# Performance work log

Hardware: AMD Instinct MI355X
Metric: run time of the kernel (lower is better)

The kernel has to match this reference:

```python
import jax, jax.numpy as jnp
import numpy as np

N_NODES = 10000
N_EDGES = 640000
D_IN = 128
D_OUT = 128


def setup_inputs() -> dict:
    key = jax.random.key(0)
    k_x, k_val, k_w, k_row, k_col = jax.random.split(key, 5)
    # Glorot init for weight, zeros for bias (matches _weight_init)
    limit = float(np.sqrt(6.0 / (D_IN + D_OUT)))
    weight = jax.random.uniform(k_w, (D_IN, D_OUT), jnp.float32, -limit, limit)
    return {
        "x": jax.random.normal(k_x, (N_NODES, D_IN), jnp.float32),
        "adj_val": jax.random.uniform(k_val, (N_EDGES,), jnp.float32),  # normalized edge weights of sparse adj
        "weight": weight,
        "bias": jnp.zeros((D_OUT,), jnp.float32),
        "adj_row": jax.random.randint(k_row, (N_EDGES,), 0, N_NODES, jnp.int32),
        "adj_col": jax.random.randint(k_col, (N_EDGES,), 0, N_NODES, jnp.int32),
    }


def reference(x, adj_val, weight, bias, adj_row, adj_col):
    # dense GEMM: h = x @ W  -> [N, D_OUT]
    h = jnp.matmul(x, weight)
    # SpMM with COO adjacency: out[r] = sum_{e: row[e]=r} val[e] * h[col[e]]
    msg = adj_val[:, None] * h[adj_col]  # [E, D_OUT] gather + scale
    out = jax.ops.segment_sum(msg, adj_row, num_segments=x.shape[0])
    return out + bias
```

## Files before the change

kernel.cpp:

```cpp
#include <hip/hip_runtime.h>

#define N_NODES 10000
#define N_EDGES 640000
#define D 128
#define NQ (N_EDGES / 4)

#define NCHUNK 64
#define QPC (NQ / NCHUNK)
#define GEMM_BLOCKS 157
#define GRID1 (NCHUNK + GEMM_BLOCKS)
#define RCAP 8
#define SPILLCAP 10000
#define CAP2 128
#define QPAD2 144
#define LSTR 136

typedef unsigned int uint32;
typedef unsigned long long u64;
typedef unsigned short u16;
typedef unsigned char u8;
using short8 = __attribute__((ext_vector_type(8))) short;
using f32x4  = __attribute__((ext_vector_type(4))) float;

__device__ __forceinline__ uint32 f2bf_bits(float f) {
    uint32 u = __float_as_uint(f);
    return (u + 0x7FFFu + ((u >> 16) & 1u)) >> 16;
}
__device__ __forceinline__ uint32 pack2(float lo, float hi) {
    return f2bf_bits(lo) | (f2bf_bits(hi) << 16);
}

__global__ __launch_bounds__(256, 4) void gemm_scatter_kernel(
    const float* __restrict__ x, const float* __restrict__ w,
    const int* __restrict__ row, const int* __restrict__ col,
    const float* __restrict__ val,
    uint32* __restrict__ h2, u8* __restrict__ cnts2,
    int* __restrict__ spillcnt, uint32* __restrict__ bstore,
    uint2* __restrict__ spill)
{
    __shared__ __align__(16) int SH[N_NODES];
    __shared__ int spillc;
    const int t = threadIdx.x;

    if (blockIdx.x < NCHUNK) {
        int* hist = SH;
        for (int i = t; i < N_NODES; i += 256) hist[i] = 0;
        if (t == 0) spillc = 0;
        __syncthreads();

        const int sb = blockIdx.x;
        const int4*   row4 = (const int4*)row;
        const int4*   col4 = (const int4*)col;
        const float4* val4 = (const float4*)val;
        const int i0 = sb * QPC;
        for (int i = i0 + t; i < i0 + QPC; i += 256) {
            int4 r = row4[i]; int4 c = col4[i]; float4 v = val4[i];
            #pragma unroll
            for (int e = 0; e < 4; ++e) {
                int rr = (e == 0) ? r.x : (e == 1) ? r.y : (e == 2) ? r.z : r.w;
                int cc = (e == 0) ? c.x : (e == 1) ? c.y : (e == 2) ? c.z : c.w;
                float vv = (e == 0) ? v.x : (e == 1) ? v.y : (e == 2) ? v.z : v.w;
                uint32 rc = (uint32)cc | (f2bf_bits(vv) << 16);
                int k = atomicAdd(&hist[rr], 1);
                if (k < RCAP)
                    bstore[(size_t)rr * (NCHUNK * RCAP) + sb * RCAP + k] = rc;
                else {
                    int ks = atomicAdd(&spillc, 1);
                    spill[(size_t)sb * SPILLCAP + ks] = make_uint2(rc, (uint32)rr);
                }
            }
        }
        __syncthreads();
        for (int r = t; r < N_NODES; r += 256) {
            int c = hist[r];
            cnts2[(size_t)sb * N_NODES + r] = (u8)((c < RCAP) ? c : RCAP);
        }
        if (t == 0) spillcnt[sb] = spillc;
    } else {
        u16* Ws = (u16*)SH;
        const int g = blockIdx.x - NCHUNK;
        const int lane = t & 63;
        const int wid  = t >> 6;
        const int q = lane >> 4, cl = lane & 15;

        const float4* w4 = (const float4*)w;
        #pragma unroll
        for (int i = 0; i < 8; ++i) {
            int lin = t + i * 256;
            int m  = lin >> 5;
            int qc = lin & 31;
            float4 r0 = w4[(2 * m) * 32 + qc];
            float4 r1 = w4[(2 * m + 1) * 32 + qc];
            int c = qc * 4;
            *(uint32*)&Ws[(c + 0) * LSTR + 2 * m] = pack2(r0.x, r1.x);
            *(uint32*)&Ws[(c + 1) * LSTR + 2 * m] = pack2(r0.y, r1.y);
            *(uint32*)&Ws[(c + 2) * LSTR + 2 * m] = pack2(r0.z, r1.z);
            *(uint32*)&Ws[(c + 3) * LSTR + 2 * m] = pack2(r0.w, r1.w);
        }

        int gr = g * 64 + wid * 16 + cl;
        if (gr >= N_NODES) gr = N_NODES - 1;
        const float* xrow = &x[(size_t)gr * D];
        float4 xv[8];
        #pragma unroll
        for (int kk = 0; kk < 4; ++kk) {
            xv[2 * kk]     = *(const float4*)&xrow[kk * 32 + q * 8];
            xv[2 * kk + 1] = *(const float4*)&xrow[kk * 32 + q * 8 + 4];
        }
        __syncthreads();

        f32x4 acc[8] = {};
        #pragma unroll
        for (int kk = 0; kk < 4; ++kk) {
            union { short8 s; uint32 u[4]; } af;
            float4 a = xv[2 * kk], b = xv[2 * kk + 1];
            af.u[0] = pack2(a.x, a.y); af.u[1] = pack2(a.z, a.w);
            af.u[2] = pack2(b.x, b.y); af.u[3] = pack2(b.z, b.w);
            #pragma unroll
            for (int ct = 0; ct < 8; ++ct) {
                short8 bf = *(const short8*)&Ws[(ct * 16 + cl) * LSTR + kk * 32 + q * 8];
                acc[ct] = __builtin_amdgcn_mfma_f32_16x16x32_bf16(af.s, bf, acc[ct], 0, 0, 0);
            }
        }
        #pragma unroll
        for (int reg = 0; reg < 4; ++reg) {
            int node = g * 64 + wid * 16 + q * 4 + reg;
            if (node < N_NODES) {
                uint32* base = h2 + (size_t)node * 64 + cl;
                #pragma unroll
                for (int ct = 0; ct < 4; ++ct)
                    base[ct * 16] = pack2(acc[ct][reg], acc[ct + 4][reg]);
            }
        }
    }
}

__global__ __launch_bounds__(256) void spmm_kernel(
    const uint32* __restrict__ bstore, const u8* __restrict__ cnts2,
    const int* __restrict__ spillcnt, const uint2* __restrict__ spill,
    const uint32* __restrict__ h2, const float* __restrict__ bias,
    float* __restrict__ out)
{
    __shared__ uint32 qbuf[8 * QPAD2];
    __shared__ u64 lcnt8[NCHUNK];
    const int t = threadIdx.x;
    const int lane = t & 63;
    const int wid  = t >> 6;
    const int r0 = blockIdx.x * 8;

    if (t < NCHUNK)
        lcnt8[t] = *(const u64*)&cnts2[(size_t)t * N_NODES + r0];
    const bool anyspill = __ballot(spillcnt[lane] != 0) != 0ull;
    __syncthreads();

    for (int half = 0; half < 2; ++half) {
        const int d = wid * 2 + half;
        const int r = r0 + d;
        uint32* qp = &qbuf[d * QPAD2];

        int c = (int)((lcnt8[lane] >> (8 * d)) & 0xFFu);
        int p = c;
        #pragma unroll
        for (int s = 1; s < 64; s <<= 1) {
            int v = __shfl_up(p, s);
            if (lane >= s) p += v;
        }
        int ntot = __shfl(p, 63);
        int base = p - c;
        const uint32* cell = &bstore[(size_t)r * (NCHUNK * RCAP) + lane * RCAP];
        uint4 c0 = {0, 0, 0, 0}, c1 = {0, 0, 0, 0};
        if (c > 0) c0 = *(const uint4*)cell;
        if (c > 4) c1 = *(const uint4*)(cell + 4);
        if (c > 0 && base + 0 < CAP2) qp[base + 0] = c0.x;
        if (c > 1 && base + 1 < CAP2) qp[base + 1] = c0.y;
        if (c > 2 && base + 2 < CAP2) qp[base + 2] = c0.z;
        if (c > 3 && base + 3 < CAP2) qp[base + 3] = c0.w;
        if (c > 4 && base + 4 < CAP2) qp[base + 4] = c1.x;
        if (c > 5 && base + 5 < CAP2) qp[base + 5] = c1.y;
        if (c > 6 && base + 6 < CAP2) qp[base + 6] = c1.z;
        if (c > 7 && base + 7 < CAP2) qp[base + 7] = c1.w;

        if (anyspill) {
            for (int ch = 0; ch < NCHUNK; ++ch) {
                int sc = spillcnt[ch];
                for (int k = 0; k < sc; ++k) {
                    uint2 e = spill[(size_t)ch * SPILLCAP + k];
                    if (e.y == (uint32)r) {
                        if (lane == 0 && ntot < CAP2) qp[ntot] = e.x;
                        ntot++;
                    }
                }
            }
        }

        float a0 = 0.f, a1 = 0.f;
        if (ntot <= CAP2) {
            if (lane < 16) qp[ntot + lane] = 0;
            __builtin_amdgcn_s_waitcnt(0);

            const int npad = (ntot + 7) & ~7;
            uint32 rq0,rq1,rq2,rq3,rq4,rq5,rq6,rq7;
            uint32 hh0,hh1,hh2,hh3,hh4,hh5,hh6,hh7;
            rq0 = qp[0]; hh0 = h2[((rq0 & 0xFFFFu) << 6) + lane];
            rq1 = qp[1]; hh1 = h2[((rq1 & 0xFFFFu) << 6) + lane];
            rq2 = qp[2]; hh2 = h2[((rq2 & 0xFFFFu) << 6) + lane];
            rq3 = qp[3]; hh3 = h2[((rq3 & 0xFFFFu) << 6) + lane];
            rq4 = qp[4]; hh4 = h2[((rq4 & 0xFFFFu) << 6) + lane];
            rq5 = qp[5]; hh5 = h2[((rq5 & 0xFFFFu) << 6) + lane];
            rq6 = qp[6]; hh6 = h2[((rq6 & 0xFFFFu) << 6) + lane];
            rq7 = qp[7]; hh7 = h2[((rq7 & 0xFFFFu) << 6) + lane];

#define CONSUME_PREFETCH(RQ, HH, P)                                          \
    {                                                                        \
        a0 = fmaf(__uint_as_float(RQ & 0xFFFF0000u),                         \
                  __uint_as_float(HH << 16), a0);                            \
        a1 = fmaf(__uint_as_float(RQ & 0xFFFF0000u),                         \
                  __uint_as_float(HH & 0xFFFF0000u), a1);                    \
        uint32 rn = qp[j + 8 + P];                                           \
        RQ = rn; HH = h2[((rn & 0xFFFFu) << 6) + lane];                      \
    }

            for (int j = 0; j < npad; j += 8) {
                CONSUME_PREFETCH(rq0, hh0, 0)
                CONSUME_PREFETCH(rq1, hh1, 1)
                CONSUME_PREFETCH(rq2, hh2, 2)
                CONSUME_PREFETCH(rq3, hh3, 3)
                CONSUME_PREFETCH(rq4, hh4, 4)
                CONSUME_PREFETCH(rq5, hh5, 5)
                CONSUME_PREFETCH(rq6, hh6, 6)
                CONSUME_PREFETCH(rq7, hh7, 7)
            }
#undef CONSUME_PREFETCH
        } else {
            for (int ch = 0; ch < NCHUNK; ++ch) {
                int c2 = (int)((lcnt8[ch] >> (8 * d)) & 0xFFu);
                for (int k = 0; k < c2; ++k) {
                    uint32 rec = bstore[(size_t)r * (NCHUNK * RCAP) + ch * RCAP + k];
                    uint32 hv = h2[((rec & 0xFFFFu) << 6) + lane];
                    a0 = fmaf(__uint_as_float(rec & 0xFFFF0000u),
                              __uint_as_float(hv << 16), a0);
                    a1 = fmaf(__uint_as_float(rec & 0xFFFF0000u),
                              __uint_as_float(hv & 0xFFFF0000u), a1);
                }
            }
            for (int ch = 0; ch < NCHUNK; ++ch) {
                int sc = spillcnt[ch];
                for (int k = 0; k < sc; ++k) {
                    uint2 e = spill[(size_t)ch * SPILLCAP + k];
                    if (e.y == (uint32)r) {
                        uint32 hv = h2[((e.x & 0xFFFFu) << 6) + lane];
                        a0 = fmaf(__uint_as_float(e.x & 0xFFFF0000u),
                                  __uint_as_float(hv << 16), a0);
                        a1 = fmaf(__uint_as_float(e.x & 0xFFFF0000u),
                                  __uint_as_float(hv & 0xFFFF0000u), a1);
                    }
                }
            }
        }

        out[(size_t)r * D + lane]      = a0 + bias[lane];
        out[(size_t)r * D + 64 + lane] = a1 + bias[lane + 64];
    }
}

extern "C" void kernel_launch(void* const* d_in, const int* in_sizes, int n_in,
                              void* d_out, int out_size, void* d_ws, size_t ws_size,
                              hipStream_t stream)
{
    const float* x    = (const float*)d_in[0];
    const float* aval = (const float*)d_in[1];
    const float* w    = (const float*)d_in[2];
    const float* bias = (const float*)d_in[3];
    const int* arow   = (const int*)d_in[4];
    const int* acol   = (const int*)d_in[5];

    char* ws = (char*)d_ws;
    uint32* h2       = (uint32*)(ws);
    u8*     cnts2    = (u8*)(ws + 2560000);
    int*    spillcnt = (int*)(ws + 3200000);
    uint32* bstore   = (uint32*)(ws + 3200512);
    uint2*  spill    = (uint2*)(ws + 23680512);

    gemm_scatter_kernel<<<GRID1, 256, 0, stream>>>(
        x, w, arow, acol, aval, h2, cnts2, spillcnt, bstore, spill);
    spmm_kernel<<<N_NODES / 8, 256, 0, stream>>>(
        bstore, cnts2, spillcnt, spill, h2, bias, (float*)d_out);
}
```

Before: 107.3 us.

## Split edge bucketing into 256 chunks and have each lane gather four chunk cells

Raises the number of scatter chunks from 64 to 256, so the first kernel runs more bucketing blocks, each handling fewer edges, and per-chunk spill capacity shrinks. In the SpMM kernel each lane now reads four chunk counts and four bucket cells, sums them for the prefix scan, and compacts their records into the shared queue, while the spill check uses a vectorized count load. The aim is more parallelism and less per-block serial work in the scatter phase. The cost is a workspace that grows from about 24 MB to about 87 MB, more count and bucket reads per row, and spill fallback loops that now walk 256 chunks.

```diff
diff --git a/kernel.cpp b/kernel.cpp
--- a/kernel.cpp
+++ b/kernel.cpp
@@ -5,12 +5,12 @@
 #define D 128
 #define NQ (N_EDGES / 4)
 
-#define NCHUNK 64
+#define NCHUNK 256
 #define QPC (NQ / NCHUNK)
 #define GEMM_BLOCKS 157
 #define GRID1 (NCHUNK + GEMM_BLOCKS)
 #define RCAP 8
-#define SPILLCAP 10000
+#define SPILLCAP 2500
 #define CAP2 128
 #define QPAD2 144
 #define LSTR 136
@@ -148,9 +148,9 @@
     const int wid  = t >> 6;
     const int r0 = blockIdx.x * 8;
 
-    if (t < NCHUNK)
-        lcnt8[t] = *(const u64*)&cnts2[(size_t)t * N_NODES + r0];
-    const bool anyspill = __ballot(spillcnt[lane] != 0) != 0ull;
+    lcnt8[t] = *(const u64*)&cnts2[(size_t)t * N_NODES + r0];
+    const int4 s4 = ((const int4*)spillcnt)[lane];
+    const bool anyspill = __ballot((s4.x | s4.y | s4.z | s4.w) != 0) != 0ull;
     __syncthreads();
 
     for (int half = 0; half < 2; ++half) {
@@ -158,7 +158,11 @@
         const int r = r0 + d;
         uint32* qp = &qbuf[d * QPAD2];
 
-        int c = (int)((lcnt8[lane] >> (8 * d)) & 0xFFu);
+        int c0 = (int)((lcnt8[lane * 4 + 0] >> (8 * d)) & 0xFFu);
+        int c1 = (int)((lcnt8[lane * 4 + 1] >> (8 * d)) & 0xFFu);
+        int c2 = (int)((lcnt8[lane * 4 + 2] >> (8 * d)) & 0xFFu);
+        int c3 = (int)((lcnt8[lane * 4 + 3] >> (8 * d)) & 0xFFu);
+        int c = c0 + c1 + c2 + c3;
         int p = c;
         #pragma unroll
         for (int s = 1; s < 64; s <<= 1) {
@@ -166,19 +170,25 @@
             if (lane >= s) p += v;
         }
         int ntot = __shfl(p, 63);
-        int base = p - c;
-        const uint32* cell = &bstore[(size_t)r * (NCHUNK * RCAP) + lane * RCAP];
-        uint4 c0 = {0, 0, 0, 0}, c1 = {0, 0, 0, 0};
-        if (c > 0) c0 = *(const uint4*)cell;
-        if (c > 4) c1 = *(const uint4*)(cell + 4);
-        if (c > 0 && base + 0 < CAP2) qp[base + 0] = c0.x;
-        if (c > 1 && base + 1 < CAP2) qp[base + 1] = c0.y;
-        if (c > 2 && base + 2 < CAP2) qp[base + 2] = c0.z;
-        if (c > 3 && base + 3 < CAP2) qp[base + 3] = c0.w;
-        if (c > 4 && base + 4 < CAP2) qp[base + 4] = c1.x;
-        if (c > 5 && base + 5 < CAP2) qp[base + 5] = c1.y;
-        if (c > 6 && base + 6 < CAP2) qp[base + 6] = c1.z;
-        if (c > 7 && base + 7 < CAP2) qp[base + 7] = c1.w;
+        const uint32* strip = &bstore[(size_t)r * (NCHUNK * RCAP) + lane * (4 * RCAP)];
+        int bo = p - c;
+        #pragma unroll
+        for (int j = 0; j < 4; ++j) {
+            int cj = (j == 0) ? c0 : (j == 1) ? c1 : (j == 2) ? c2 : c3;
+            const uint32* cell = strip + j * RCAP;
+            uint4 v0 = {0, 0, 0, 0}, v1 = {0, 0, 0, 0};
+            if (cj > 0) v0 = *(const uint4*)cell;
+            if (cj > 4) v1 = *(const uint4*)(cell + 4);
+            if (cj > 0 && bo + 0 < CAP2) qp[bo + 0] = v0.x;
+            if (cj > 1 && bo + 1 < CAP2) qp[bo + 1] = v0.y;
+            if (cj > 2 && bo + 2 < CAP2) qp[bo + 2] = v0.z;
+            if (cj > 3 && bo + 3 < CAP2) qp[bo + 3] = v0.w;
+            if (cj > 4 && bo + 4 < CAP2) qp[bo + 4] = v1.x;
+            if (cj > 5 && bo + 5 < CAP2) qp[bo + 5] = v1.y;
+            if (cj > 6 && bo + 6 < CAP2) qp[bo + 6] = v1.z;
+            if (cj > 7 && bo + 7 < CAP2) qp[bo + 7] = v1.w;
+            bo += cj;
+        }
 
         if (anyspill) {
             for (int ch = 0; ch < NCHUNK; ++ch) {
@@ -233,8 +243,8 @@
 #undef CONSUME_PREFETCH
         } else {
             for (int ch = 0; ch < NCHUNK; ++ch) {
-                int c2 = (int)((lcnt8[ch] >> (8 * d)) & 0xFFu);
-                for (int k = 0; k < c2; ++k) {
+                int c2v = (int)((lcnt8[ch] >> (8 * d)) & 0xFFu);
+                for (int k = 0; k < c2v; ++k) {
                     uint32 rec = bstore[(size_t)r * (NCHUNK * RCAP) + ch * RCAP + k];
                     uint32 hv = h2[((rec & 0xFFFFu) << 6) + lane];
                     a0 = fmaf(__uint_as_float(rec & 0xFFFF0000u),
@@ -277,9 +287,9 @@
     char* ws = (char*)d_ws;
     uint32* h2       = (uint32*)(ws);
     u8*     cnts2    = (u8*)(ws + 2560000);
-    int*    spillcnt = (int*)(ws + 3200000);
-    uint32* bstore   = (uint32*)(ws + 3200512);
-    uint2*  spill    = (uint2*)(ws + 23680512);
+    int*    spillcnt = (int*)(ws + 5120000);
+    uint32* bstore   = (uint32*)(ws + 5121024);
+    uint2*  spill    = (uint2*)(ws + 87041024);
 
     gemm_scatter_kernel<<<GRID1, 256, 0, stream>>>(
         x, w, arow, acol, aval, h2, cnts2, spillcnt, bstore, spill);
```

New measurement: 104.7 us. 2.4% less time.

## Bucket edges by row with global atomic cursors instead of per-chunk LDS histograms

Applied to the files above, without the earlier changes.

Replaces the 64 chunked scatter blocks, which kept per-chunk LDS histograms and fixed 8-slot cells, with 512 grid-stride blocks. These append each edge into a per-row region of 112 slots using global atomics on padded cursors, with a single global spill list. The SpMM kernel then reads a contiguous per-row list and no longer needs the prefix scan over 64 chunk counts, and the large LDS histogram is gone from the GEMM blocks. The cost is a memset before launch, contended global atomics, and a linear scan of the spill list by every row whenever any spill occurs.

```diff
diff --git a/kernel.cpp b/kernel.cpp
--- a/kernel.cpp
+++ b/kernel.cpp
@@ -5,12 +5,13 @@
 #define D 128
 #define NQ (N_EDGES / 4)
 
-#define NCHUNK 64
-#define QPC (NQ / NCHUNK)
+#define NSCAT 512
 #define GEMM_BLOCKS 157
-#define GRID1 (NCHUNK + GEMM_BLOCKS)
-#define RCAP 8
-#define SPILLCAP 10000
+#define GRID1 (NSCAT + GEMM_BLOCKS)
+#define REGCAP 112
+#define RSTRIDE 128
+#define CSTRIDE 16
+#define SPILLCAP 4096
 #define CAP2 128
 #define QPAD2 144
 #define LSTR 136
@@ -18,7 +19,6 @@
 typedef unsigned int uint32;
 typedef unsigned long long u64;
 typedef unsigned short u16;
-typedef unsigned char u8;
 using short8 = __attribute__((ext_vector_type(8))) short;
 using f32x4  = __attribute__((ext_vector_type(4))) float;
 
@@ -34,26 +34,20 @@
     const float* __restrict__ x, const float* __restrict__ w,
     const int* __restrict__ row, const int* __restrict__ col,
     const float* __restrict__ val,
-    uint32* __restrict__ h2, u8* __restrict__ cnts2,
-    int* __restrict__ spillcnt, uint32* __restrict__ bstore,
+    uint32* __restrict__ h2, int* __restrict__ cursor,
+    int* __restrict__ spillcnt, uint32* __restrict__ region,
     uint2* __restrict__ spill)
 {
-    __shared__ __align__(16) int SH[N_NODES];
-    __shared__ int spillc;
+    __shared__ __align__(16) u16 Ws[128 * LSTR];
     const int t = threadIdx.x;
 
-    if (blockIdx.x < NCHUNK) {
-        int* hist = SH;
-        for (int i = t; i < N_NODES; i += 256) hist[i] = 0;
-        if (t == 0) spillc = 0;
-        __syncthreads();
-
-        const int sb = blockIdx.x;
+    if (blockIdx.x < NSCAT) {
+        const int tid = blockIdx.x * 256 + t;
+        const int stride = NSCAT * 256;
         const int4*   row4 = (const int4*)row;
         const int4*   col4 = (const int4*)col;
         const float4* val4 = (const float4*)val;
-        const int i0 = sb * QPC;
-        for (int i = i0 + t; i < i0 + QPC; i += 256) {
+        for (int i = tid; i < NQ; i += stride) {
             int4 r = row4[i]; int4 c = col4[i]; float4 v = val4[i];
             #pragma unroll
             for (int e = 0; e < 4; ++e) {
@@ -61,24 +55,17 @@
                 int cc = (e == 0) ? c.x : (e == 1) ? c.y : (e == 2) ? c.z : c.w;
                 float vv = (e == 0) ? v.x : (e == 1) ? v.y : (e == 2) ? v.z : v.w;
                 uint32 rc = (uint32)cc | (f2bf_bits(vv) << 16);
-                int k = atomicAdd(&hist[rr], 1);
-                if (k < RCAP)
-                    bstore[(size_t)rr * (NCHUNK * RCAP) + sb * RCAP + k] = rc;
+                int pos = atomicAdd(&cursor[rr * CSTRIDE], 1);
+                if (pos < REGCAP)
+                    region[(size_t)rr * RSTRIDE + pos] = rc;
                 else {
-                    int ks = atomicAdd(&spillc, 1);
-                    spill[(size_t)sb * SPILLCAP + ks] = make_uint2(rc, (uint32)rr);
+                    int o = atomicAdd(spillcnt, 1);
+                    if (o < SPILLCAP) spill[o] = make_uint2((uint32)rr, rc);
                 }
             }
         }
-        __syncthreads();
-        for (int r = t; r < N_NODES; r += 256) {
-            int c = hist[r];
-            cnts2[(size_t)sb * N_NODES + r] = (u8)((c < RCAP) ? c : RCAP);
-        }
-        if (t == 0) spillcnt[sb] = spillc;
     } else {
-        u16* Ws = (u16*)SH;
-        const int g = blockIdx.x - NCHUNK;
+        const int g = blockIdx.x - NSCAT;
         const int lane = t & 63;
         const int wid  = t >> 6;
         const int q = lane >> 4, cl = lane & 15;
@@ -136,59 +123,43 @@
 }
 
 __global__ __launch_bounds__(256) void spmm_kernel(
-    const uint32* __restrict__ bstore, const u8* __restrict__ cnts2,
+    const uint32* __restrict__ region, const int* __restrict__ cursor,
     const int* __restrict__ spillcnt, const uint2* __restrict__ spill,
     const uint32* __restrict__ h2, const float* __restrict__ bias,
     float* __restrict__ out)
 {
     __shared__ uint32 qbuf[8 * QPAD2];
-    __shared__ u64 lcnt8[NCHUNK];
+    __shared__ int cnt8[8];
     const int t = threadIdx.x;
     const int lane = t & 63;
     const int wid  = t >> 6;
     const int r0 = blockIdx.x * 8;
 
-    if (t < NCHUNK)
-        lcnt8[t] = *(const u64*)&cnts2[(size_t)t * N_NODES + r0];
-    const bool anyspill = __ballot(spillcnt[lane] != 0) != 0ull;
+    if (t < 8) {
+        int c = cursor[(r0 + t) * CSTRIDE];
+        cnt8[t] = (c < REGCAP) ? c : REGCAP;
+    }
+    int nsp = spillcnt[0];
+    if (nsp > SPILLCAP) nsp = SPILLCAP;
     __syncthreads();
 
     for (int half = 0; half < 2; ++half) {
         const int d = wid * 2 + half;
         const int r = r0 + d;
         uint32* qp = &qbuf[d * QPAD2];
-
-        int c = (int)((lcnt8[lane] >> (8 * d)) & 0xFFu);
-        int p = c;
-        #pragma unroll
-        for (int s = 1; s < 64; s <<= 1) {
-            int v = __shfl_up(p, s);
-            if (lane >= s) p += v;
-        }
-        int ntot = __shfl(p, 63);
-        int base = p - c;
-        const uint32* cell = &bstore[(size_t)r * (NCHUNK * RCAP) + lane * RCAP];
-        uint4 c0 = {0, 0, 0, 0}, c1 = {0, 0, 0, 0};
-        if (c > 0) c0 = *(const uint4*)cell;
-        if (c > 4) c1 = *(const uint4*)(cell + 4);
-        if (c > 0 && base + 0 < CAP2) qp[base + 0] = c0.x;
-        if (c > 1 && base + 1 < CAP2) qp[base + 1] = c0.y;
-        if (c > 2 && base + 2 < CAP2) qp[base + 2] = c0.z;
-        if (c > 3 && base + 3 < CAP2) qp[base + 3] = c0.w;
-        if (c > 4 && base + 4 < CAP2) qp[base + 4] = c1.x;
-        if (c > 5 && base + 5 < CAP2) qp[base + 5] = c1.y;
-        if (c > 6 && base + 6 < CAP2) qp[base + 6] = c1.z;
-        if (c > 7 && base + 7 < CAP2) qp[base + 7] = c1.w;
-
-        if (anyspill) {
-            for (int ch = 0; ch < NCHUNK; ++ch) {
-                int sc = spillcnt[ch];
-                for (int k = 0; k < sc; ++k) {
-                    uint2 e = spill[(size_t)ch * SPILLCAP + k];
-                    if (e.y == (uint32)r) {
-                        if (lane == 0 && ntot < CAP2) qp[ntot] = e.x;
-                        ntot++;
-                    }
+        int cnt = cnt8[d];
+
+        uint2 rv = *(const uint2*)&region[(size_t)r * RSTRIDE + 2 * lane];
+        if (2 * lane     < cnt) qp[2 * lane]     = rv.x;
+        if (2 * lane + 1 < cnt) qp[2 * lane + 1] = rv.y;
+        int ntot = cnt;
+
+        if (nsp > 0) {
+            for (int k = 0; k < nsp; ++k) {
+                uint2 e = spill[k];
+                if (e.x == (uint32)r) {
+                    if (lane == 0 && ntot < CAP2) qp[ntot] = e.y;
+                    ntot++;
                 }
             }
         }
@@ -232,28 +203,22 @@
             }
 #undef CONSUME_PREFETCH
         } else {
-            for (int ch = 0; ch < NCHUNK; ++ch) {
-                int c2 = (int)((lcnt8[ch] >> (8 * d)) & 0xFFu);
-                for (int k = 0; k < c2; ++k) {
-                    uint32 rec = bstore[(size_t)r * (NCHUNK * RCAP) + ch * RCAP + k];
-                    uint32 hv = h2[((rec & 0xFFFFu) << 6) + lane];
-                    a0 = fmaf(__uint_as_float(rec & 0xFFFF0000u),
+            for (int k = 0; k < cnt; ++k) {
+                uint32 rec = region[(size_t)r * RSTRIDE + k];
+                uint32 hv = h2[((rec & 0xFFFFu) << 6) + lane];
+                a0 = fmaf(__uint_as_float(rec & 0xFFFF0000u),
+                          __uint_as_float(hv << 16), a0);
+                a1 = fmaf(__uint_as_float(rec & 0xFFFF0000u),
+                          __uint_as_float(hv & 0xFFFF0000u), a1);
+            }
+            for (int k = 0; k < nsp; ++k) {
+                uint2 e = spill[k];
+                if (e.x == (uint32)r) {
+                    uint32 hv = h2[((e.y & 0xFFFFu) << 6) + lane];
+                    a0 = fmaf(__uint_as_float(e.y & 0xFFFF0000u),
                               __uint_as_float(hv << 16), a0);
-                    a1 = fmaf(__uint_as_float(rec & 0xFFFF0000u),
+                    a1 = fmaf(__uint_as_float(e.y & 0xFFFF0000u),
                               __uint_as_float(hv & 0xFFFF0000u), a1);
-                }
-            }
-            for (int ch = 0; ch < NCHUNK; ++ch) {
-                int sc = spillcnt[ch];
-                for (int k = 0; k < sc; ++k) {
-                    uint2 e = spill[(size_t)ch * SPILLCAP + k];
-                    if (e.y == (uint32)r) {
-                        uint32 hv = h2[((e.x & 0xFFFFu) << 6) + lane];
-                        a0 = fmaf(__uint_as_float(e.x & 0xFFFF0000u),
-                                  __uint_as_float(hv << 16), a0);
-                        a1 = fmaf(__uint_as_float(e.x & 0xFFFF0000u),
-                                  __uint_as_float(hv & 0xFFFF0000u), a1);
-                    }
                 }
             }
         }
@@ -276,13 +241,15 @@
 
     char* ws = (char*)d_ws;
     uint32* h2       = (uint32*)(ws);
-    u8*     cnts2    = (u8*)(ws + 2560000);
+    int*    cursor   = (int*)(ws + 2560000);
     int*    spillcnt = (int*)(ws + 3200000);
-    uint32* bstore   = (uint32*)(ws + 3200512);
-    uint2*  spill    = (uint2*)(ws + 23680512);
+    uint2*  spill    = (uint2*)(ws + 3200064);
+    uint32* region   = (uint32*)(ws + 3232832);
+
+    hipMemsetAsync(ws + 2560000, 0, 640064, stream);
 
     gemm_scatter_kernel<<<GRID1, 256, 0, stream>>>(
-        x, w, arow, acol, aval, h2, cnts2, spillcnt, bstore, spill);
+        x, w, arow, acol, aval, h2, cursor, spillcnt, region, spill);
     spmm_kernel<<<N_NODES / 8, 256, 0, stream>>>(
-        bstore, cnts2, spillcnt, spill, h2, bias, (float*)d_out);
-}
+        region, cursor, spillcnt, spill, h2, bias, (float*)d_out);
+}
```

Result: slower. 114.3 us (+6.6%).
